# Optimization experiments

Measured on AMD Instinct MI355X. Metric: run time of the kernel, lower is better.

Reference implementation:

```python
import jax, jax.numpy as jnp
import numpy as np

B, T, D, U = 4096, 50, 128, 128  # batch, history len, embed dim, GRU units (U==D)
ATT_H1, ATT_H2 = 128, 64         # Attention MLP hiddens (hard-coded in source)
DH1, DH2 = 256, 128              # deep model hiddens
BN_EPS = 1e-3
LEAKY = 0.0003


def setup_inputs() -> dict:
    key = jax.random.key(0)
    ks = iter(jax.random.split(key, 40))
    n = lambda shape, s=0.05: jax.random.normal(next(ks), shape, dtype=jnp.float32) * s
    DI = U + D  # deep_input dim
    return {
        "inputs": n((B, T + 1, D), 1.0),
        # Keras GRU (reset_after=True): kernel, recurrent kernel, bias[2,3U] (input/recurrent)
        "gru_W": n((D, 3 * U)), "gru_U": n((U, 3 * U)), "gru_b": n((2, 3 * U)),
        # Attention MLP: input is concat([h, news-h, news, h*news]) -> 4U
        "att_W1": n((4 * U, ATT_H1)), "att_b1": n((ATT_H1,)),
        "att_W2": n((ATT_H1, ATT_H2)), "att_b2": n((ATT_H2,)),
        "att_W3": n((ATT_H2, 1)), "att_b3": n((1,)),
        # AUGRU Bilinear gates: Dense(U, bias) on inputs, Dense(U, no bias) on state
        "au_Wu": n((U, U)), "au_bu": n((U,)), "au_Uu": n((U, U)),
        "au_Wr": n((U, U)), "au_br": n((U,)), "au_Ur": n((U, U)),
        "au_Wc": n((U, U)), "au_bc": n((U,)), "au_Uc": n((U, U)),
        # deep model: BN (inference) + 2 leaky-relu Dense + sigmoid head
        "bn_gamma": jnp.ones((DI,), jnp.float32), "bn_beta": jnp.zeros((DI,), jnp.float32),
        "bn_mean": jnp.zeros((DI,), jnp.float32), "bn_var": jnp.ones((DI,), jnp.float32),
        "d_W1": n((DI, DH1)), "d_b1": n((DH1,)),
        "d_W2": n((DH1, DH2)), "d_b2": n((DH2,)),
        "f_W": n((DH2, 1)), "f_b": n((1,)),
    }


def _gru(x_seq, W, Ur, b):
    # Keras GRU, reset_after=True, gate order [z, r, h]
    Xp = jnp.einsum('btd,dk->btk', x_seq, W) + b[0]  # precompute input projections
    h0 = jnp.zeros((x_seq.shape[0], Ur.shape[0]), x_seq.dtype)

    def step(h, xp):
        hp = h @ Ur + b[1]
        xz, xr, xh = jnp.split(xp, 3, axis=-1)
        hz, hr, hh = jnp.split(hp, 3, axis=-1)
        z = jax.nn.sigmoid(xz + hz)
        r = jax.nn.sigmoid(xr + hr)
        hc = jnp.tanh(xh + r * hh)
        hn = z * h + (1.0 - z) * hc
        return hn, hn

    _, hs = jax.lax.scan(step, h0, jnp.swapaxes(Xp, 0, 1))
    return jnp.swapaxes(hs, 0, 1)  # [B,T,U]


def reference(inputs, gru_W, gru_U, gru_b,
              att_W1, att_b1, att_W2, att_b2, att_W3, att_b3,
              au_Wu, au_bu, au_Uu, au_Wr, au_br, au_Ur, au_Wc, au_bc, au_Uc,
              bn_gamma, bn_beta, bn_mean, bn_var,
              d_W1, d_b1, d_W2, d_b2, f_W, f_b):
    hist = inputs[:, :-1, :]   # [B,T,D]
    news = inputs[:, -1, :]    # [B,D]

    hs = _gru(hist, gru_W, gru_U, gru_b)  # [B,T,U]

    # Attention (vectorized over the per-timestep Python loop; same math)
    news_b = jnp.broadcast_to(news[:, None, :], hs.shape)
    emb = jnp.concatenate([hs, news_b - hs, news_b, hs * news_b], axis=-1)  # [B,T,4U]
    a = jax.nn.relu(jnp.einsum('bti,ij->btj', emb, att_W1) + att_b1)
    a = jax.nn.relu(jnp.einsum('bti,ij->btj', a, att_W2) + att_b2)
    ats = jax.nn.sigmoid(jnp.einsum('bti,ij->btj', a, att_W3) + att_b3)  # [B,T,1]

    # AUGRU: precompute input-side projections, scan the recurrence
    xu = jnp.einsum('btd,dk->btk', hs, au_Wu) + au_bu
    xr = jnp.einsum('btd,dk->btk', hs, au_Wr) + au_br
    xc = jnp.einsum('btd,dk->btk', hs, au_Wc) + au_bc

    def au_step(h, xs):
        xu_t, xr_t, xc_t, at_t = xs
        u = jax.nn.sigmoid(xu_t + h @ au_Uu)
        r = jax.nn.sigmoid(xr_t + h @ au_Ur)
        c = jnp.tanh(xc_t + r * (h @ au_Uc))
        u_ = at_t * u
        hn = (1.0 - u_) * h + u_ * c
        return hn, None

    h0 = jnp.zeros_like(hs[:, 0, :])
    xs = (jnp.swapaxes(xu, 0, 1), jnp.swapaxes(xr, 0, 1),
          jnp.swapaxes(xc, 0, 1), jnp.swapaxes(ats, 0, 1))
    h_final, _ = jax.lax.scan(au_step, h0, xs)

    # deep model: BN (inference) -> Dense + leaky ReLU x2 -> sigmoid head
    x = jnp.concatenate([h_final, news], axis=-1)
    x = (x - bn_mean) * jax.lax.rsqrt(bn_var + BN_EPS) * bn_gamma + bn_beta
    x = x @ d_W1 + d_b1
    x = jnp.where(x >= 0, x, LEAKY * x)
    x = x @ d_W2 + d_b2
    x = jnp.where(x >= 0, x, LEAKY * x)
    y = jax.nn.sigmoid(x @ f_W + f_b)  # [B,1]
    return y
```

## Files before the change

kernel.cpp:

```cpp
#include <hip/hip_runtime.h>
#include <hip/hip_bf16.h>
#include <math.h>


#define LK 0.0003f

typedef __attribute__((ext_vector_type(8))) short short8;
typedef __attribute__((ext_vector_type(4))) float f32x4;

union U8 { short8 s; unsigned short u[8]; };

__device__ __forceinline__ float sigf(float x) {
    return __builtin_amdgcn_rcpf(1.0f + __expf(-x));
}
__device__ __forceinline__ float tanhfast(float x) {
    return fmaf(2.0f, __builtin_amdgcn_rcpf(1.0f + __expf(-2.0f * x)), -1.0f);
}
__device__ __forceinline__ float lky(float v) { return v >= 0.0f ? v : LK * v; }
__device__ __forceinline__ unsigned short f2bf(float f) {
    __bf16 b = (__bf16)f;
    return *reinterpret_cast<unsigned short*>(&b);
}
__device__ __forceinline__ unsigned pk2(float a, float b) {
    return (unsigned)f2bf(a) | ((unsigned)f2bf(b) << 16);
}
__device__ __forceinline__ float bf2f(unsigned short h) {
    return __uint_as_float(((unsigned)h) << 16);
}
__device__ __forceinline__ int swz(int row, int kbyte, int stride) {
    return row * stride + (kbyte ^ ((row & 7) << 4));
}
__device__ __forceinline__ f32x4 mfma16(short8 a, short8 b, f32x4 c) {
    return __builtin_amdgcn_mfma_f32_16x16x32_bf16(a, b, c, 0, 0, 0);
}

__global__ void pack_all(
    const float* __restrict__ gW, const float* __restrict__ gU,
    const float* __restrict__ aWu, const float* __restrict__ aWr, const float* __restrict__ aWc,
    const float* __restrict__ aUu, const float* __restrict__ aUr, const float* __restrict__ aUc,
    const float* __restrict__ tW1, const float* __restrict__ tW2,
    const float* __restrict__ dW1, const float* __restrict__ dW2,
    const float* __restrict__ abu, const float* __restrict__ abr, const float* __restrict__ abc,
    unsigned short* __restrict__ Wg, unsigned short* __restrict__ Ug,
    unsigned short* __restrict__ Wau, unsigned short* __restrict__ Uau,
    unsigned short* __restrict__ WA, unsigned short* __restrict__ WN,
    unsigned short* __restrict__ AW2,
    unsigned short* __restrict__ DW1, unsigned short* __restrict__ DW2,
    float* __restrict__ bp)
{
    int i = blockIdx.x * 256 + threadIdx.x;
    if (i < 49152) {
        int n = i >> 7, k = i & 127;
        Wg[i] = f2bf(gW[k * 384 + n]);
        Ug[i] = f2bf(gU[k * 384 + n]);
    } else if (i < 98304) {
        int j = i - 49152; int n = j >> 7, k = j & 127;
        int g = n >> 7, c = n & 127;
        const float* s = (g == 0) ? aWu : (g == 1) ? aWr : aWc;
        const float* u = (g == 0) ? aUu : (g == 1) ? aUr : aUc;
        Wau[j] = f2bf(s[k * 128 + c]);
        Uau[j] = f2bf(u[k * 128 + c]);
    } else if (i < 131072) {
        int j = i - 98304; int n = j >> 8, k = j & 255;
        float v = (k < 128) ? (tW1[k * 128 + n] - tW1[(128 + k) * 128 + n])
                            : tW1[(384 + (k - 128)) * 128 + n];
        WA[j] = f2bf(v);
    } else if (i < 147456) {
        int j = i - 131072; int n = j >> 7, k = j & 127;
        WN[j] = f2bf(tW1[(128 + k) * 128 + n] + tW1[(256 + k) * 128 + n]);
    } else if (i < 155648) {
        int j = i - 147456; int n = j >> 7, k = j & 127;
        AW2[j] = f2bf(tW2[k * 64 + n]);
    } else if (i < 221184) {
        int j = i - 155648; int n = j >> 8, k = j & 255;
        DW1[j] = f2bf(dW1[k * 256 + n]);
    } else if (i < 253952) {
        int j = i - 221184; int n = j >> 8, k = j & 255;
        DW2[j] = f2bf(dW2[k * 128 + n]);
    } else if (i < 254336) {
        int j = i - 253952;
        bp[j] = (j < 128) ? abu[j] : (j < 256) ? abr[j - 128] : abc[j - 256];
    }
}

__global__ __launch_bounds__(512, 2) void nterm_kernel(
    const float* __restrict__ inputs, const unsigned short* __restrict__ WN,
    const float* __restrict__ b1, float* __restrict__ nterm)
{
    __shared__ __align__(16) unsigned char nb[64 * 256];

    const int tid = threadIdx.x;
    const int wv = tid >> 6, l = tid & 63, l15 = l & 15, lg = l >> 4;
    const size_t b0 = (size_t)blockIdx.x * 64;

    {
        int r = tid >> 3, c = tid & 7;
        const float* src = inputs + ((b0 + r) * 51 + 50) * 128 + c * 16;
        float4 v0 = *(const float4*)(src);
        float4 v1 = *(const float4*)(src + 4);
        float4 v2 = *(const float4*)(src + 8);
        float4 v3 = *(const float4*)(src + 12);
        *(uint4*)(nb + swz(r, c * 32, 256)) =
            make_uint4(pk2(v0.x, v0.y), pk2(v0.z, v0.w), pk2(v1.x, v1.y), pk2(v1.z, v1.w));
        *(uint4*)(nb + swz(r, c * 32 + 16, 256)) =
            make_uint4(pk2(v2.x, v2.y), pk2(v2.z, v2.w), pk2(v3.x, v3.y), pk2(v3.z, v3.w));
    }
    __syncthreads();

    short8 wf[4];
#pragma unroll
    for (int kt = 0; kt < 4; ++kt)
        wf[kt] = *(const short8*)(WN + (wv * 16 + l15) * 128 + kt * 32 + lg * 8);

    f32x4 acc[4];
#pragma unroll
    for (int rt = 0; rt < 4; ++rt) acc[rt] = (f32x4){0.f, 0.f, 0.f, 0.f};
#pragma unroll
    for (int rt = 0; rt < 4; ++rt)
#pragma unroll
        for (int kt = 0; kt < 4; ++kt) {
            short8 axx = *(const short8*)(nb + swz(rt * 16 + l15, kt * 64 + lg * 16, 256));
            acc[rt] = mfma16(axx, wf[kt], acc[rt]);
        }
    float bb = b1[wv * 16 + l15];
#pragma unroll
    for (int rt = 0; rt < 4; ++rt)
#pragma unroll
        for (int j = 0; j < 4; ++j)
            nterm[(b0 + rt * 16 + lg * 4 + j) * 128 + wv * 16 + l15] = acc[rt][j] + bb;
}

__global__ __launch_bounds__(512, 2) void gru_attn(
    const float* __restrict__ inputs, const unsigned short* __restrict__ Wt,
    const unsigned short* __restrict__ Ut, const float* __restrict__ gb,
    const unsigned short* __restrict__ WA, const unsigned short* __restrict__ AW2,
    const float* __restrict__ ab2, const float* __restrict__ nterm,
    const float* __restrict__ W3, const float* __restrict__ b3,
    unsigned short* __restrict__ hs, float* __restrict__ ats)
{
    __shared__ __align__(16) unsigned char xbuf[2][4096];
    __shared__ __align__(16) unsigned char hbuf[2][4096];
    __shared__ __align__(16) unsigned char pbuf[2][4096];
    __shared__ __align__(16) unsigned char a1buf[2][4096];
    __shared__ float a2buf[2][16 * 64];
    __shared__ float w3l[64];

    const int tid = threadIdx.x;
    const int wv = tid >> 6, l = tid & 63, l15 = l & 15, lg = l >> 4;
    const size_t row0 = (size_t)blockIdx.x * 16;
    const int ucol = wv * 16 + l15;

    short8 wf[3][4], uf[3][4];
#pragma unroll
    for (int g = 0; g < 3; ++g)
#pragma unroll
        for (int kt = 0; kt < 4; ++kt) {
            int n = g * 128 + ucol;
            int k0 = kt * 32 + lg * 8;
            wf[g][kt] = *(const short8*)(Wt + n * 128 + k0);
            uf[g][kt] = *(const short8*)(Ut + n * 128 + k0);
        }
    short8 waf[8];
#pragma unroll
    for (int kt = 0; kt < 8; ++kt)
        waf[kt] = *(const short8*)(WA + ucol * 256 + kt * 32 + lg * 8);
    short8 w2f[4];
    const int n2 = (wv & 3) * 16 + l15;
    if (wv < 4) {
#pragma unroll
        for (int kt = 0; kt < 4; ++kt)
            w2f[kt] = *(const short8*)(AW2 + n2 * 128 + kt * 32 + lg * 8);
    }
    const float b2v = (wv < 4) ? ab2[n2] : 0.f;
    const float b3v = b3[0];
    if (tid < 64) w3l[tid] = W3[tid];

    const float bx2 = gb[256 + ucol], bh2 = gb[640 + ucol];
    const float bz  = gb[ucol] + gb[384 + ucol];
    const float br  = gb[128 + ucol] + gb[512 + ucol];

    float nt4[4], news4[4];
    size_t hsbase[4];
#pragma unroll
    for (int j = 0; j < 4; ++j) {
        int m = lg * 4 + j;
        nt4[j]   = nterm[(row0 + m) * 128 + ucol];
        news4[j] = inputs[((row0 + m) * 51 + 50) * 128 + ucol];
        hsbase[j] = ((row0 + m) * 50) * 128 + ucol;
    }

    const int sr = tid >> 5, ss = tid & 31;

    *(uint2*)(hbuf[0] + tid * 8) = make_uint2(0u, 0u);
    {
        float4 v = *(const float4*)&inputs[((row0 + sr) * 51) * 128 + ss * 4];
        *(uint2*)(xbuf[0] + swz(sr, ss * 8, 256)) = make_uint2(pk2(v.x, v.y), pk2(v.z, v.w));
    }
    float hreg[4] = {0.f, 0.f, 0.f, 0.f};
    __syncthreads();

    for (int t = 0; t <= 52; ++t) {
        const int p = t & 1;

        float4 xpf;
        if (t < 49) xpf = *(const float4*)&inputs[((row0 + sr) * 51 + (t + 1)) * 128 + ss * 4];

        short8 ah[4];
        if (t <= 50) {
#pragma unroll
            for (int kt = 0; kt < 4; ++kt)
                ah[kt] = *(const short8*)(hbuf[p] + swz(l15, kt * 64 + lg * 16, 256));
        }

        if (t < 50) {
            short8 ax[4];
#pragma unroll
            for (int kt = 0; kt < 4; ++kt)
                ax[kt] = *(const short8*)(xbuf[p] + swz(l15, kt * 64 + lg * 16, 256));
            f32x4 accx[3], acch[3];
#pragma unroll
            for (int g = 0; g < 3; ++g) {
                accx[g] = (f32x4){0.f, 0.f, 0.f, 0.f};
                acch[g] = (f32x4){0.f, 0.f, 0.f, 0.f};
            }
#pragma unroll
            for (int kt = 0; kt < 4; ++kt)
#pragma unroll
                for (int g = 0; g < 3; ++g) {
                    accx[g] = mfma16(ax[kt], wf[g][kt], accx[g]);
                    acch[g] = mfma16(ah[kt], uf[g][kt], acch[g]);
                }
#pragma unroll
            for (int j = 0; j < 4; ++j) {
                int m = lg * 4 + j;
                float z  = sigf(accx[0][j] + acch[0][j] + bz);
                float r  = sigf(accx[1][j] + acch[1][j] + br);
                float hc = tanhfast(accx[2][j] + bx2 + r * (acch[2][j] + bh2));
                float hn = fmaf(z, hreg[j] - hc, hc);
                hreg[j] = hn;
                unsigned short hb = f2bf(hn);
                *(unsigned short*)(hbuf[p ^ 1] + swz(m, ucol * 2, 256)) = hb;
                *(unsigned short*)(pbuf[p ^ 1] + swz(m, ucol * 2, 256)) = f2bf(hn * news4[j]);
                hs[hsbase[j] + (size_t)t * 128] = hb;
            }
        }

        if (t >= 1 && t <= 50) {
            short8 pa[4];
#pragma unroll
            for (int kt = 0; kt < 4; ++kt)
                pa[kt] = *(const short8*)(pbuf[p] + swz(l15, kt * 64 + lg * 16, 256));
            f32x4 lacc = (f32x4){0.f, 0.f, 0.f, 0.f};
#pragma unroll
            for (int kt = 0; kt < 4; ++kt) lacc = mfma16(ah[kt], waf[kt], lacc);
#pragma unroll
            for (int kt = 0; kt < 4; ++kt) lacc = mfma16(pa[kt], waf[4 + kt], lacc);
#pragma unroll
            for (int j = 0; j < 4; ++j) {
                float v = fmaxf(lacc[j] + nt4[j], 0.f);
                *(unsigned short*)(a1buf[p] + swz(lg * 4 + j, ucol * 2, 256)) = f2bf(v);
            }
        }

        if (t >= 2 && t <= 51 && wv < 4) {
            f32x4 c2 = (f32x4){0.f, 0.f, 0.f, 0.f};
#pragma unroll
            for (int kt = 0; kt < 4; ++kt) {
                short8 aa = *(const short8*)(a1buf[p ^ 1] + swz(l15, kt * 64 + lg * 16, 256));
                c2 = mfma16(aa, w2f[kt], c2);
            }
#pragma unroll
            for (int j = 0; j < 4; ++j)
                a2buf[p][(lg * 4 + j) * 64 + n2] = fmaxf(c2[j] + b2v, 0.f);
        }

        if (t >= 3 && tid < 256) {
            int rrow = tid >> 5, cc = tid & 31;
            const float* a2r = &a2buf[p ^ 1][rrow * 64];
            float s = a2r[cc] * w3l[cc] + a2r[cc + 32] * w3l[cc + 32];
            s += __shfl_xor(s, 16, 32);
            s += __shfl_xor(s, 8, 32);
            s += __shfl_xor(s, 4, 32);
            s += __shfl_xor(s, 2, 32);
            s += __shfl_xor(s, 1, 32);
            if ((tid & 31) == 0) ats[(row0 + rrow) * 50 + (t - 3)] = sigf(s + b3v);
        }

        if (t < 49)
            *(uint2*)(xbuf[p ^ 1] + swz(sr, ss * 8, 256)) =
                make_uint2(pk2(xpf.x, xpf.y), pk2(xpf.z, xpf.w));
        __syncthreads();
    }
}

__global__ __launch_bounds__(512, 2) void augru_mfma(
    const unsigned short* __restrict__ hsrc, const unsigned short* __restrict__ Wt,
    const unsigned short* __restrict__ Ut, const float* __restrict__ bp,
    const float* __restrict__ ats, float* __restrict__ hf)
{
    __shared__ __align__(16) unsigned char xbuf[2][4096];
    __shared__ __align__(16) unsigned char hbuf[2][4096];
    __shared__ float atsl[16 * 50];

    const int tid = threadIdx.x;
    const int wv = tid >> 6, l = tid & 63, l15 = l & 15, lg = l >> 4;
    const size_t row0 = (size_t)blockIdx.x * 16;
    const int ucol = wv * 16 + l15;

    short8 wf[3][4], uf[3][4];
#pragma unroll
    for (int g = 0; g < 3; ++g)
#pragma unroll
        for (int kt = 0; kt < 4; ++kt) {
            int n = g * 128 + ucol;
            int k0 = kt * 32 + lg * 8;
            wf[g][kt] = *(const short8*)(Wt + n * 128 + k0);
            uf[g][kt] = *(const short8*)(Ut + n * 128 + k0);
        }
    const float bx0 = bp[ucol], bx1 = bp[128 + ucol], bx2 = bp[256 + ucol];

    const int sr = tid >> 5, ss = tid & 31;

    *(uint2*)(hbuf[0] + tid * 8) = make_uint2(0u, 0u);
    if (tid < 400) {
        atsl[tid] = ats[row0 * 50 + tid];
        atsl[tid + 400] = ats[row0 * 50 + tid + 400];
    }
    {
        uint2 v = *(const uint2*)(hsrc + ((row0 + sr) * 50) * 128 + ss * 4);
        *(uint2*)(xbuf[0] + swz(sr, ss * 8, 256)) = v;
    }
    float hreg[4] = {0.f, 0.f, 0.f, 0.f};
    __syncthreads();

    for (int t = 0; t < 50; ++t) {
        const int p = t & 1;
        uint2 xnext;
        if (t < 49) xnext = *(const uint2*)(hsrc + ((row0 + sr) * 50 + t + 1) * 128 + ss * 4);

        short8 ax[4], ah[4];
#pragma unroll
        for (int kt = 0; kt < 4; ++kt) {
            int off = swz(l15, kt * 64 + lg * 16, 256);
            ax[kt] = *(const short8*)(xbuf[p] + off);
            ah[kt] = *(const short8*)(hbuf[p] + off);
        }
        f32x4 accx[3], acch[3];
#pragma unroll
        for (int g = 0; g < 3; ++g) {
            accx[g] = (f32x4){0.f, 0.f, 0.f, 0.f};
            acch[g] = (f32x4){0.f, 0.f, 0.f, 0.f};
        }
#pragma unroll
        for (int kt = 0; kt < 4; ++kt)
#pragma unroll
            for (int g = 0; g < 3; ++g) {
                accx[g] = mfma16(ax[kt], wf[g][kt], accx[g]);
                acch[g] = mfma16(ah[kt], uf[g][kt], acch[g]);
            }
#pragma unroll
        for (int j = 0; j < 4; ++j) {
            int m = lg * 4 + j;
            float u  = sigf(accx[0][j] + bx0 + acch[0][j]);
            float r  = sigf(accx[1][j] + bx1 + acch[1][j]);
            float c  = tanhfast(accx[2][j] + bx2 + r * acch[2][j]);
            float uu = atsl[m * 50 + t] * u;
            float hn = fmaf(uu, c - hreg[j], hreg[j]);
            hreg[j] = hn;
            *(unsigned short*)(hbuf[p ^ 1] + swz(m, ucol * 2, 256)) = f2bf(hn);
        }
        if (t < 49) *(uint2*)(xbuf[p ^ 1] + swz(sr, ss * 8, 256)) = xnext;
        __syncthreads();
    }
#pragma unroll
    for (int j = 0; j < 4; ++j)
        hf[(row0 + lg * 4 + j) * 128 + ucol] = hreg[j];
}

__global__ __launch_bounds__(256, 2) void final_mfma(
    const float* __restrict__ hfv, const float* __restrict__ inputs,
    const float* __restrict__ gam, const float* __restrict__ bet,
    const float* __restrict__ mu, const float* __restrict__ var,
    const unsigned short* __restrict__ W1t, const float* __restrict__ b1,
    const unsigned short* __restrict__ W2t, const float* __restrict__ b2,
    const float* __restrict__ fW, const float* __restrict__ fb,
    float* __restrict__ out)
{
    __shared__ __align__(16) unsigned char xnb[16 * 512];
    __shared__ __align__(16) unsigned char d1b[16 * 512];
    __shared__ float d2b[16 * 132];
    __shared__ float wfl[128];

    const int tid = threadIdx.x;
    const int wv = tid >> 6, l = tid & 63, l15 = l & 15, lg = l >> 4;
    const size_t r0 = (size_t)blockIdx.x * 16;

    short8 w1f[4][8];
#pragma unroll
    for (int p = 0; p < 4; ++p)
#pragma unroll
        for (int kt = 0; kt < 8; ++kt) {
            int n = wv * 64 + p * 16 + l15;
            w1f[p][kt] = *(const short8*)(W1t + n * 256 + kt * 32 + lg * 8);
        }
    short8 w2f[2][8];
#pragma unroll
    for (int p = 0; p < 2; ++p)
#pragma unroll
        for (int kt = 0; kt < 8; ++kt) {
            int n = wv * 32 + p * 16 + l15;
            w2f[p][kt] = *(const short8*)(W2t + n * 256 + kt * 32 + lg * 8);
        }
    if (tid < 128) wfl[tid] = fW[tid];

    {
        int r = tid >> 4, c = tid & 15, k0 = c * 16;
        float v[16];
#pragma unroll
        for (int q = 0; q < 16; ++q) {
            int k = k0 + q;
            float x = (k < 128) ? hfv[(r0 + r) * 128 + k]
                                : inputs[((r0 + r) * 51 + 50) * 128 + (k - 128)];
            float s = gam[k] * rsqrtf(var[k] + 0.001f);
            v[q] = (x - mu[k]) * s + bet[k];
        }
        *(uint4*)(xnb + swz(r, k0 * 2, 512)) =
            make_uint4(pk2(v[0], v[1]), pk2(v[2], v[3]), pk2(v[4], v[5]), pk2(v[6], v[7]));
        *(uint4*)(xnb + swz(r, k0 * 2 + 16, 512)) =
            make_uint4(pk2(v[8], v[9]), pk2(v[10], v[11]), pk2(v[12], v[13]), pk2(v[14], v[15]));
    }
    __syncthreads();

    f32x4 a1[4];
#pragma unroll
    for (int p = 0; p < 4; ++p) a1[p] = (f32x4){0.f, 0.f, 0.f, 0.f};
#pragma unroll
    for (int kt = 0; kt < 8; ++kt) {
        short8 axx = *(const short8*)(xnb + swz(l15, kt * 64 + lg * 16, 512));
#pragma unroll
        for (int p = 0; p < 4; ++p) a1[p] = mfma16(axx, w1f[p][kt], a1[p]);
    }
#pragma unroll
    for (int p = 0; p < 4; ++p) {
        float bb = b1[wv * 64 + p * 16 + l15];
#pragma unroll
        for (int j = 0; j < 4; ++j) {
            int row = lg * 4 + j, col = wv * 64 + p * 16 + l15;
            *(unsigned short*)(d1b + swz(row, col * 2, 512)) = f2bf(lky(a1[p][j] + bb));
        }
    }
    __syncthreads();

    f32x4 a2[2];
#pragma unroll
    for (int p = 0; p < 2; ++p) a2[p] = (f32x4){0.f, 0.f, 0.f, 0.f};
#pragma unroll
    for (int kt = 0; kt < 8; ++kt) {
        short8 axx = *(const short8*)(d1b + swz(l15, kt * 64 + lg * 16, 512));
#pragma unroll
        for (int p = 0; p < 2; ++p) a2[p] = mfma16(axx, w2f[p][kt], a2[p]);
    }
#pragma unroll
    for (int p = 0; p < 2; ++p) {
        float bb = b2[wv * 32 + p * 16 + l15];
#pragma unroll
        for (int j = 0; j < 4; ++j)
            d2b[(lg * 4 + j) * 132 + wv * 32 + p * 16 + l15] = lky(a2[p][j] + bb);
    }
    __syncthreads();

    if (tid < 16) {
        float s = fb[0];
#pragma unroll 8
        for (int k = 0; k < 128; ++k) s += d2b[tid * 132 + k] * wfl[k];
        out[r0 + tid] = sigf(s);
    }
}

extern "C" void kernel_launch(void* const* d_in, const int* in_sizes, int n_in,
                              void* d_out, int out_size, void* d_ws, size_t ws_size,
                              hipStream_t stream)
{
    const float* inputs   = (const float*)d_in[0];
    const float* gru_W    = (const float*)d_in[1];
    const float* gru_U    = (const float*)d_in[2];
    const float* gru_b    = (const float*)d_in[3];
    const float* att_W1   = (const float*)d_in[4];
    const float* att_b1   = (const float*)d_in[5];
    const float* att_W2   = (const float*)d_in[6];
    const float* att_b2   = (const float*)d_in[7];
    const float* att_W3   = (const float*)d_in[8];
    const float* att_b3   = (const float*)d_in[9];
    const float* au_Wu    = (const float*)d_in[10];
    const float* au_bu    = (const float*)d_in[11];
    const float* au_Uu    = (const float*)d_in[12];
    const float* au_Wr    = (const float*)d_in[13];
    const float* au_br    = (const float*)d_in[14];
    const float* au_Ur    = (const float*)d_in[15];
    const float* au_Wc    = (const float*)d_in[16];
    const float* au_bc    = (const float*)d_in[17];
    const float* au_Uc    = (const float*)d_in[18];
    const float* bn_gamma = (const float*)d_in[19];
    const float* bn_beta  = (const float*)d_in[20];
    const float* bn_mean  = (const float*)d_in[21];
    const float* bn_var   = (const float*)d_in[22];
    const float* d_W1     = (const float*)d_in[23];
    const float* d_b1     = (const float*)d_in[24];
    const float* d_W2     = (const float*)d_in[25];
    const float* d_b2     = (const float*)d_in[26];
    const float* f_W      = (const float*)d_in[27];
    const float* f_b      = (const float*)d_in[28];

    char* w = (char*)d_ws;
    unsigned short* hs  = (unsigned short*)w;
    float* ats          = (float*)(w + 52428800);
    float* hf           = (float*)(w + 53248000);
    float* nterm        = (float*)(w + 55345152);
    unsigned short* Wg  = (unsigned short*)(w + 57442304);
    unsigned short* Ug  = (unsigned short*)(w + 57540608);
    unsigned short* Wau = (unsigned short*)(w + 57638912);
    unsigned short* Uau = (unsigned short*)(w + 57737216);
    unsigned short* WA  = (unsigned short*)(w + 57835520);
    unsigned short* WN  = (unsigned short*)(w + 57901056);
    unsigned short* AW2 = (unsigned short*)(w + 57933824);
    unsigned short* DW1 = (unsigned short*)(w + 57950208);
    unsigned short* DW2 = (unsigned short*)(w + 58081280);
    float* bp           = (float*)(w + 58146816);

    pack_all<<<994, 256, 0, stream>>>(
        gru_W, gru_U, au_Wu, au_Wr, au_Wc, au_Uu, au_Ur, au_Uc,
        att_W1, att_W2, d_W1, d_W2, au_bu, au_br, au_bc,
        Wg, Ug, Wau, Uau, WA, WN, AW2, DW1, DW2, bp);
    nterm_kernel<<<64, 512, 0, stream>>>(inputs, WN, att_b1, nterm);
    gru_attn<<<256, 512, 0, stream>>>(inputs, Wg, Ug, gru_b, WA, AW2, att_b2,
                                      nterm, att_W3, att_b3, hs, ats);
    augru_mfma<<<256, 512, 0, stream>>>(hs, Wau, Uau, bp, ats, hf);
    final_mfma<<<256, 256, 0, stream>>>(hf, inputs, bn_gamma, bn_beta, bn_mean, bn_var,
                                        DW1, d_b1, DW2, d_b2, f_W, f_b, (float*)d_out);
}
```

Before: 170.7 us.

## Batch input prefetch four steps ahead and coalesce hs stores via LDS

In the GRU+attention kernel and the AUGRU kernel, the per-step global load of the next input row becomes a batched load of four future timesteps into registers every fourth step. This puts more latency slack before each value is needed. The GRU kernel also stops issuing scattered 2-byte global stores of the hidden state. It reads the freshly written hbuf row back as 8-byte chunks and flushes four timesteps at once as coalesced stores. The attention reduction moves from threads 0-255 to threads 256-511 to spread work across waves. The cost is more live registers, which could hurt occupancy under the launch bounds.

```diff
diff --git a/kernel.cpp b/kernel.cpp
--- a/kernel.cpp
+++ b/kernel.cpp
@@ -180,30 +180,48 @@
     const float br  = gb[128 + ucol] + gb[512 + ucol];
 
     float nt4[4], news4[4];
-    size_t hsbase[4];
 #pragma unroll
     for (int j = 0; j < 4; ++j) {
         int m = lg * 4 + j;
         nt4[j]   = nterm[(row0 + m) * 128 + ucol];
         news4[j] = inputs[((row0 + m) * 51 + 50) * 128 + ucol];
-        hsbase[j] = ((row0 + m) * 50) * 128 + ucol;
     }
 
     const int sr = tid >> 5, ss = tid & 31;
+    const float* xsrc = inputs + (row0 + sr) * 51 * 128 + ss * 4;
+    unsigned short* hdst = hs + (row0 + sr) * 50 * 128 + ss * 4;
 
     *(uint2*)(hbuf[0] + tid * 8) = make_uint2(0u, 0u);
     {
-        float4 v = *(const float4*)&inputs[((row0 + sr) * 51) * 128 + ss * 4];
+        float4 v = *(const float4*)(xsrc);
         *(uint2*)(xbuf[0] + swz(sr, ss * 8, 256)) = make_uint2(pk2(v.x, v.y), pk2(v.z, v.w));
     }
     float hreg[4] = {0.f, 0.f, 0.f, 0.f};
+    float4 xr4[4];
+    uint2 hsb[4];
     __syncthreads();
 
     for (int t = 0; t <= 52; ++t) {
         const int p = t & 1;
 
-        float4 xpf;
-        if (t < 49) xpf = *(const float4*)&inputs[((row0 + sr) * 51 + (t + 1)) * 128 + ss * 4];
+        if ((t & 3) == 0 && t < 49) {
+#pragma unroll
+            for (int k = 0; k < 4; ++k)
+                if (t + 1 + k < 50)
+                    xr4[k] = *(const float4*)(xsrc + (size_t)(t + 1 + k) * 128);
+        }
+
+        if (t >= 1 && t <= 50) {
+            hsb[(t - 1) & 3] = *(const uint2*)(hbuf[p] + swz(sr, ss * 8, 256));
+            if (t >= 4 && (t & 3) == 0) {
+#pragma unroll
+                for (int k = 0; k < 4; ++k)
+                    *(uint2*)(hdst + (size_t)(t - 4 + k) * 128) = hsb[k];
+            } else if (t == 50) {
+                *(uint2*)(hdst + (size_t)48 * 128) = hsb[0];
+                *(uint2*)(hdst + (size_t)49 * 128) = hsb[1];
+            }
+        }
 
         short8 ah[4];
         if (t <= 50) {
@@ -238,10 +256,8 @@
                 float hc = tanhfast(accx[2][j] + bx2 + r * (acch[2][j] + bh2));
                 float hn = fmaf(z, hreg[j] - hc, hc);
                 hreg[j] = hn;
-                unsigned short hb = f2bf(hn);
-                *(unsigned short*)(hbuf[p ^ 1] + swz(m, ucol * 2, 256)) = hb;
+                *(unsigned short*)(hbuf[p ^ 1] + swz(m, ucol * 2, 256)) = f2bf(hn);
                 *(unsigned short*)(pbuf[p ^ 1] + swz(m, ucol * 2, 256)) = f2bf(hn * news4[j]);
-                hs[hsbase[j] + (size_t)t * 128] = hb;
             }
         }
 
@@ -274,8 +290,8 @@
                 a2buf[p][(lg * 4 + j) * 64 + n2] = fmaxf(c2[j] + b2v, 0.f);
         }
 
-        if (t >= 3 && tid < 256) {
-            int rrow = tid >> 5, cc = tid & 31;
+        if (t >= 3 && tid >= 256) {
+            int rrow = (tid - 256) >> 5, cc = tid & 31;
             const float* a2r = &a2buf[p ^ 1][rrow * 64];
             float s = a2r[cc] * w3l[cc] + a2r[cc + 32] * w3l[cc + 32];
             s += __shfl_xor(s, 16, 32);
@@ -286,9 +302,11 @@
             if ((tid & 31) == 0) ats[(row0 + rrow) * 50 + (t - 3)] = sigf(s + b3v);
         }
 
-        if (t < 49)
+        if (t < 49) {
+            float4 xv = xr4[t & 3];
             *(uint2*)(xbuf[p ^ 1] + swz(sr, ss * 8, 256)) =
-                make_uint2(pk2(xpf.x, xpf.y), pk2(xpf.z, xpf.w));
+                make_uint2(pk2(xv.x, xv.y), pk2(xv.z, xv.w));
+        }
         __syncthreads();
     }
 }
@@ -320,6 +338,7 @@
     const float bx0 = bp[ucol], bx1 = bp[128 + ucol], bx2 = bp[256 + ucol];
 
     const int sr = tid >> 5, ss = tid & 31;
+    const unsigned short* xsrc = hsrc + (row0 + sr) * 50 * 128 + ss * 4;
 
     *(uint2*)(hbuf[0] + tid * 8) = make_uint2(0u, 0u);
     if (tid < 400) {
@@ -327,16 +346,21 @@
         atsl[tid + 400] = ats[row0 * 50 + tid + 400];
     }
     {
-        uint2 v = *(const uint2*)(hsrc + ((row0 + sr) * 50) * 128 + ss * 4);
+        uint2 v = *(const uint2*)(xsrc);
         *(uint2*)(xbuf[0] + swz(sr, ss * 8, 256)) = v;
     }
     float hreg[4] = {0.f, 0.f, 0.f, 0.f};
+    uint2 xb[4];
     __syncthreads();
 
     for (int t = 0; t < 50; ++t) {
         const int p = t & 1;
-        uint2 xnext;
-        if (t < 49) xnext = *(const uint2*)(hsrc + ((row0 + sr) * 50 + t + 1) * 128 + ss * 4);
+        if ((t & 3) == 0 && t < 49) {
+#pragma unroll
+            for (int k = 0; k < 4; ++k)
+                if (t + 1 + k < 50)
+                    xb[k] = *(const uint2*)(xsrc + (size_t)(t + 1 + k) * 128);
+        }
 
         short8 ax[4], ah[4];
 #pragma unroll
@@ -369,7 +393,7 @@
             hreg[j] = hn;
             *(unsigned short*)(hbuf[p ^ 1] + swz(m, ucol * 2, 256)) = f2bf(hn);
         }
-        if (t < 49) *(uint2*)(xbuf[p ^ 1] + swz(sr, ss * 8, 256)) = xnext;
+        if (t < 49) *(uint2*)(xbuf[p ^ 1] + swz(sr, ss * 8, 256)) = xb[t & 3];
         __syncthreads();
     }
 #pragma unroll
```

New measurement: 237.5 us. +39.1%, slower.
